# Kernel tuning notes

Measured on AMD Instinct MI355X. Metric: run time of the kernel, lower is better.

Reference implementation:

```python
import jax, jax.numpy as jnp
import numpy as np

N_HEADS = 4
D_K = 64


def setup_inputs() -> dict:
    key = jax.random.key(0)
    k1, k2, k3, k4, k5 = jax.random.split(key, 5)
    C = 256
    return {
        "x": jax.random.normal(k1, (16, C, 32, 32), dtype=jnp.float32),
        "W_qkv": jax.random.normal(k2, (C, N_HEADS * D_K * 3), dtype=jnp.float32) * (C ** -0.5),
        "b_qkv": jax.random.normal(k3, (N_HEADS * D_K * 3,), dtype=jnp.float32) * 0.02,
        "W_out": jax.random.normal(k4, (N_HEADS * D_K, C), dtype=jnp.float32) * ((N_HEADS * D_K) ** -0.5),
        "b_out": jax.random.normal(k5, (C,), dtype=jnp.float32) * 0.02,
    }


def reference(x, W_qkv, b_qkv, W_out, b_out):
    # NOTE: the original forward never applies self.norm and ignores t.
    B, C, H, W = x.shape
    N = H * W
    scale = D_K ** -0.5
    xf = x.reshape(B, C, N).transpose(0, 2, 1)            # [B, N, C]
    qkv = (xf @ W_qkv + b_qkv).reshape(B, N, N_HEADS, 3 * D_K)
    q, k, v = jnp.split(qkv, 3, axis=-1)                  # each [B, N, H, dk]
    attn = jnp.einsum('bihd,bjhd->bijh', q, k) * scale    # [B, N, N, H]
    attn = jax.nn.softmax(attn, axis=2)                   # softmax over keys (j)
    res = jnp.einsum('bijh,bjhd->bihd', attn, v)          # [B, N, H, dk]
    res = res.reshape(B, N, N_HEADS * D_K)
    res = res @ W_out + b_out + xf                        # residual on flattened x
    return res.transpose(0, 2, 1).reshape(B, C, H, W)
```

## Files before the change

### kernel.cpp

```cpp
#include <hip/hip_runtime.h>
#include <math.h>

#define NN 1024

typedef __attribute__((ext_vector_type(8))) __bf16 bf16x8;
typedef __attribute__((ext_vector_type(4))) __bf16 bf16x4;
typedef __attribute__((ext_vector_type(4))) float f32x4;

__device__ __forceinline__ unsigned short f2bf(float f) {
    __bf16 h = (__bf16)f;
    return *(unsigned short*)&h;
}
__device__ __forceinline__ ushort4 pack4(float a, float b, float c, float d) {
    bf16x4 v;
    v[0] = (__bf16)a; v[1] = (__bf16)b; v[2] = (__bf16)c; v[3] = (__bf16)d;
    return *(ushort4*)&v;
}
__device__ __forceinline__ float bf2f(unsigned short u) {
    unsigned v = (unsigned)u << 16;
    return __uint_as_float(v);
}

__device__ __forceinline__ void async_cp16(const unsigned short* g, unsigned short* l) {
    __builtin_amdgcn_global_load_lds(
        (const __attribute__((address_space(1))) unsigned int*)g,
        (__attribute__((address_space(3))) unsigned int*)l,
        16, 0, 0);
}

__global__ __launch_bounds__(256) void prep_transpose(
    const float* __restrict__ x, const float* __restrict__ Wq,
    const float* __restrict__ Wo,
    unsigned short* __restrict__ xb, unsigned short* __restrict__ Wqt,
    unsigned short* __restrict__ Wot)
{
    __shared__ __align__(16) unsigned short T[64 * 72];
    const int bx = blockIdx.x;
    const int rt = blockIdx.y;
    const float* src; unsigned short* dst; int ncol, c0;
    if (bx < 256) {
        int b = bx >> 4; int ct = bx & 15;
        src = x + (size_t)b * 256 * 1024; dst = xb + (size_t)b * 1024 * 256;
        ncol = 1024; c0 = ct * 64;
    } else if (bx < 268) {
        src = Wq; dst = Wqt; ncol = 768; c0 = (bx - 256) * 64;
    } else {
        src = Wo; dst = Wot; ncol = 256; c0 = (bx - 268) * 64;
    }
    const int t = threadIdx.x;
    #pragma unroll
    for (int i = 0; i < 4; ++i) {
        int r  = i * 16 + (t >> 4);
        int c4 = (t & 15) * 4;
        float4 v = *(const float4*)&src[(size_t)(rt * 64 + r) * ncol + c0 + c4];
        *(ushort4*)&T[r * 72 + c4] = pack4(v.x, v.y, v.z, v.w);
    }
    __syncthreads();
    #pragma unroll
    for (int i = 0; i < 2; ++i) {
        int task = t + 256 * i;
        int c = task & 63, rs = task >> 6;
        ushort u8[8];
        #pragma unroll
        for (int k = 0; k < 8; ++k) u8[k] = T[(rs * 8 + k) * 72 + c];
        *(uint4*)&dst[(size_t)(c0 + c) * 256 + rt * 64 + rs * 8] = *(uint4*)u8;
    }
}

__global__ __launch_bounds__(256, 4) void qkv_gemm(
    const unsigned short* __restrict__ xb, const unsigned short* __restrict__ Wqt,
    const float* __restrict__ bias,
    unsigned short* __restrict__ Qb, unsigned short* __restrict__ Kb,
    unsigned short* __restrict__ Vtb)
{
    __shared__ __align__(16) unsigned short As[128 * 40];
    __shared__ __align__(16) unsigned short Bs[128 * 40];
    const int jt = blockIdx.x;
    const int m0 = blockIdx.y * 128;
    const int b  = m0 >> 10;
    const int n0 = m0 & 1023;
    const int t = threadIdx.x;
    const int w = t >> 6, lane = t & 63, quad = lane >> 4, cc = lane & 15;
    const int wm = (w & 1) * 64;
    const int wj = (w >> 1) * 64;

    f32x4 acc[4][4];
    #pragma unroll
    for (int ms = 0; ms < 4; ++ms)
        #pragma unroll
        for (int js = 0; js < 4; ++js) acc[ms][js] = (f32x4)(0.f);

    for (int k0 = 0; k0 < 256; k0 += 32) {
        __syncthreads();
        #pragma unroll
        for (int i = 0; i < 2; ++i) {
            int flat = t + 256 * i;
            int row = flat >> 2, seg = flat & 3;
            *(uint4*)&As[row * 40 + seg * 8] =
                *(const uint4*)&xb[(size_t)(m0 + row) * 256 + k0 + seg * 8];
            *(uint4*)&Bs[row * 40 + seg * 8] =
                *(const uint4*)&Wqt[(size_t)(jt * 128 + row) * 256 + k0 + seg * 8];
        }
        __syncthreads();
        bf16x8 af[4], bfr[4];
        #pragma unroll
        for (int ms = 0; ms < 4; ++ms)
            af[ms] = *(bf16x8*)&As[(wm + ms * 16 + cc) * 40 + quad * 8];
        #pragma unroll
        for (int js = 0; js < 4; ++js)
            bfr[js] = *(bf16x8*)&Bs[(wj + js * 16 + cc) * 40 + quad * 8];
        #pragma unroll
        for (int ms = 0; ms < 4; ++ms)
            #pragma unroll
            for (int js = 0; js < 4; ++js)
                acc[ms][js] = __builtin_amdgcn_mfma_f32_16x16x32_bf16(
                    af[ms], bfr[js], acc[ms][js], 0, 0, 0);
    }

    const int chunk = jt * 2 + (w >> 1);
    const int h = chunk / 3, type = chunk % 3;
    const size_t bh = (size_t)b * 4 + h;
    float bias_r[4];
    #pragma unroll
    for (int js = 0; js < 4; ++js) bias_r[js] = bias[jt * 128 + wj + js * 16 + cc];

    if (type == 2) {
        #pragma unroll
        for (int ms = 0; ms < 4; ++ms)
            #pragma unroll
            for (int js = 0; js < 4; ++js) {
                int dd = js * 16 + cc;
                int n = n0 + wm + ms * 16 + quad * 4;
                *(ushort4*)&Vtb[(bh * 64 + dd) * NN + n] =
                    pack4(acc[ms][js][0] + bias_r[js], acc[ms][js][1] + bias_r[js],
                          acc[ms][js][2] + bias_r[js], acc[ms][js][3] + bias_r[js]);
            }
    } else {
        unsigned short* dst = type ? Kb : Qb;
        const float sc = type ? 1.0f : 0.18033688011112042f;
        #pragma unroll
        for (int ms = 0; ms < 4; ++ms)
            #pragma unroll
            for (int js = 0; js < 4; ++js)
                #pragma unroll
                for (int r = 0; r < 4; ++r) {
                    int n = n0 + wm + ms * 16 + quad * 4 + r;
                    dst[(bh * NN + n) * 64 + js * 16 + cc] =
                        f2bf((acc[ms][js][r] + bias_r[js]) * sc);
                }
    }
}

__global__ __launch_bounds__(256, 4) void flash_attn(
    const unsigned short* __restrict__ Qb, const unsigned short* __restrict__ Kb,
    const unsigned short* __restrict__ Vtb, unsigned short* __restrict__ resb)
{
    __shared__ __align__(16) unsigned short QP[4096];
    __shared__ __align__(16) unsigned short Ks0[4096];
    __shared__ __align__(16) unsigned short Ks1[4096];
    __shared__ __align__(16) unsigned short Vt0[4096];
    __shared__ __align__(16) unsigned short Vt1[4096];

    const int blk = blockIdx.x;
    const int qt = blk & 15;
    const int h  = (blk >> 4) & 3;
    const int b  = blk >> 6;
    const int t  = threadIdx.x;
    const int w  = t >> 6;
    const int lane = t & 63;
    const int quad = lane >> 4;
    const int c    = lane & 15;

    const size_t bh = (size_t)(b * 4 + h);
    const unsigned short* Qg = Qb  + bh * NN * 64;
    const unsigned short* Kg = Kb  + bh * NN * 64;
    const unsigned short* Vg = Vtb + bh * 64 * NN;

    #pragma unroll
    for (int i = 0; i < 2; ++i) {
        int f = i * 256 + t;
        int row = f >> 3;
        int gc  = (f & 7) ^ (row & 7);
        async_cp16(&Qg[(size_t)(qt * 64 + row) * 64 + gc * 8], &QP[f * 8]);
        async_cp16(&Kg[(size_t)row * 64 + gc * 8], &Ks0[f * 8]);
        async_cp16(&Vg[(size_t)row * NN + gc * 8], &Vt0[f * 8]);
    }
    __syncthreads();

    bf16x8 qf[2];
    #pragma unroll
    for (int ks = 0; ks < 2; ++ks) {
        int sc_ = (ks * 4 + quad) ^ (c & 7);
        qf[ks] = *(bf16x8*)&QP[((w * 16 + c) * 8 + sc_) * 8];
    }

    float l_part = 0.f;
    f32x4 O[4];
    #pragma unroll
    for (int dt = 0; dt < 4; ++dt) O[dt] = (f32x4)(0.f);

    auto step = [&](int kt, const unsigned short* curK, const unsigned short* curV,
                    unsigned short* nxtK, unsigned short* nxtV,
                    bool pref, bool bar) {
        if (bar) __syncthreads();
        if (pref) {
            int ktn = kt + 1;
            #pragma unroll
            for (int i = 0; i < 2; ++i) {
                int f = i * 256 + t;
                int row = f >> 3;
                int gc  = (f & 7) ^ (row & 7);
                async_cp16(&Kg[(size_t)(ktn * 64 + row) * 64 + gc * 8], &nxtK[f * 8]);
                async_cp16(&Vg[(size_t)row * NN + ktn * 64 + gc * 8], &nxtV[f * 8]);
            }
        }

        f32x4 S[4];
        #pragma unroll
        for (int jt = 0; jt < 4; ++jt) S[jt] = (f32x4)(0.f);
        #pragma unroll
        for (int ks = 0; ks < 2; ++ks) {
            #pragma unroll
            for (int jt = 0; jt < 4; ++jt) {
                int sc_ = (ks * 4 + quad) ^ (c & 7);
                bf16x8 kf = *(bf16x8*)&curK[((jt * 16 + c) * 8 + sc_) * 8];
                S[jt] = __builtin_amdgcn_mfma_f32_16x16x32_bf16(kf, qf[ks], S[jt], 0, 0, 0);
            }
        }

        float p[4][4], rsj[4];
        #pragma unroll
        for (int jt = 0; jt < 4; ++jt) {
            #pragma unroll
            for (int r = 0; r < 4; ++r)
                p[jt][r] = __builtin_amdgcn_exp2f(S[jt][r]);
            rsj[jt] = (p[jt][0] + p[jt][1]) + (p[jt][2] + p[jt][3]);
        }
        l_part += (rsj[0] + rsj[1]) + (rsj[2] + rsj[3]);

        #pragma unroll
        for (int jt = 0; jt < 4; ++jt) {
            int scw = (jt * 2 + (quad >> 1)) ^ (c & 7);
            *(ushort4*)&QP[(w * 16 + c) * 64 + scw * 8 + (quad & 1) * 4] =
                pack4(p[jt][0], p[jt][1], p[jt][2], p[jt][3]);
        }

        #pragma unroll
        for (int js = 0; js < 2; ++js) {
            int scp = (js * 4 + quad) ^ (c & 7);
            bf16x8 pf = *(bf16x8*)&QP[(w * 16 + c) * 64 + scp * 8];
            #pragma unroll
            for (int dt = 0; dt < 4; ++dt) {
                int sc_ = (js * 4 + quad) ^ (c & 7);
                bf16x8 vf = *(bf16x8*)&curV[((dt * 16 + c) * 8 + sc_) * 8];
                O[dt] = __builtin_amdgcn_mfma_f32_16x16x32_bf16(pf, vf, O[dt], 0, 0, 0);
            }
        }
    };

    step(0, Ks0, Vt0, Ks1, Vt1, true, false);
    for (int kt2 = 0; kt2 < 7; ++kt2) {
        int kt = 2 * kt2 + 1;
        step(kt,     Ks1, Vt1, Ks0, Vt0, true, true);
        step(kt + 1, Ks0, Vt0, Ks1, Vt1, true, true);
    }
    step(15, Ks1, Vt1, Ks0, Vt0, false, true);

    float l_tot = l_part;
    l_tot += __shfl_xor(l_tot, 16);
    l_tot += __shfl_xor(l_tot, 32);

    float linv[4];
    #pragma unroll
    for (int r = 0; r < 4; ++r) linv[r] = 1.f / __shfl(l_tot, quad * 4 + r);
    #pragma unroll
    for (int dt = 0; dt < 4; ++dt)
        #pragma unroll
        for (int r = 0; r < 4; ++r) {
            int row = qt * 64 + w * 16 + quad * 4 + r;
            resb[((size_t)(b * NN + row)) * 256 + h * 64 + dt * 16 + c] =
                f2bf(O[dt][r] * linv[r]);
        }
}

__global__ __launch_bounds__(256, 4) void out_gemm(
    const unsigned short* __restrict__ resb, const unsigned short* __restrict__ Wot,
    const float* __restrict__ bias, const unsigned short* __restrict__ xb,
    float* __restrict__ out)
{
    __shared__ __align__(16) unsigned short As[64 * 40];
    __shared__ __align__(16) unsigned short Bs[64 * 40];
    const int n0 = blockIdx.x * 64;
    const int c0 = blockIdx.y * 64;
    const int b  = blockIdx.z;
    const int t = threadIdx.x;
    const int w = t >> 6, lane = t & 63, quad = lane >> 4, cc = lane & 15;
    const int wm = (w & 1) * 32;
    const int wj = (w >> 1) * 32;

    f32x4 acc[2][2];
    #pragma unroll
    for (int ms = 0; ms < 2; ++ms)
        #pragma unroll
        for (int js = 0; js < 2; ++js) acc[ms][js] = (f32x4)(0.f);

    for (int k0 = 0; k0 < 256; k0 += 32) {
        __syncthreads();
        {
            int r = t >> 2, seg = t & 3;
            *(uint4*)&As[r * 40 + seg * 8] =
                *(const uint4*)&resb[((size_t)b * NN + n0 + r) * 256 + k0 + seg * 8];
            *(uint4*)&Bs[r * 40 + seg * 8] =
                *(const uint4*)&Wot[(size_t)(c0 + r) * 256 + k0 + seg * 8];
        }
        __syncthreads();
        bf16x8 af[2], bfr[2];
        #pragma unroll
        for (int ms = 0; ms < 2; ++ms)
            af[ms] = *(bf16x8*)&As[(wm + ms * 16 + cc) * 40 + quad * 8];
        #pragma unroll
        for (int js = 0; js < 2; ++js)
            bfr[js] = *(bf16x8*)&Bs[(wj + js * 16 + cc) * 40 + quad * 8];
        #pragma unroll
        for (int ms = 0; ms < 2; ++ms)
            #pragma unroll
            for (int js = 0; js < 2; ++js)
                acc[ms][js] = __builtin_amdgcn_mfma_f32_16x16x32_bf16(
                    af[ms], bfr[js], acc[ms][js], 0, 0, 0);
    }

    #pragma unroll
    for (int js = 0; js < 2; ++js) {
        int cI = c0 + wj + js * 16 + cc;
        float bi = bias[cI];
        #pragma unroll
        for (int ms = 0; ms < 2; ++ms) {
            int n = n0 + wm + ms * 16 + quad * 4;
            size_t off = ((size_t)b * 256 + cI) * NN + n;
            float4 o;
            float* op = &o.x;
            #pragma unroll
            for (int r = 0; r < 4; ++r) {
                float xr = bf2f(xb[((size_t)b * NN + n + r) * 256 + cI]);
                op[r] = acc[ms][js][r] + bi + xr;
            }
            *(float4*)&out[off] = o;
        }
    }
}

extern "C" void kernel_launch(void* const* d_in, const int* in_sizes, int n_in,
                              void* d_out, int out_size, void* d_ws, size_t ws_size,
                              hipStream_t stream)
{
    const float* x     = (const float*)d_in[0];
    const float* W_qkv = (const float*)d_in[1];
    const float* b_qkv = (const float*)d_in[2];
    const float* W_out = (const float*)d_in[3];
    const float* b_out = (const float*)d_in[4];
    float* out = (float*)d_out;

    char* wsc = (char*)d_ws;
    unsigned short* xb   = (unsigned short*)(wsc);
    unsigned short* Wqt  = (unsigned short*)(wsc + ((size_t)8 << 20));
    unsigned short* Wot  = (unsigned short*)(wsc + ((size_t)8 << 20) + ((size_t)512 << 10));
    unsigned short* Qb   = (unsigned short*)(wsc + ((size_t)9  << 20));
    unsigned short* Kb   = (unsigned short*)(wsc + ((size_t)17 << 20));
    unsigned short* Vtb  = (unsigned short*)(wsc + ((size_t)25 << 20));
    unsigned short* resb = (unsigned short*)(wsc + ((size_t)33 << 20));

    prep_transpose<<<dim3(272, 4), 256, 0, stream>>>(x, W_qkv, W_out, xb, Wqt, Wot);
    qkv_gemm<<<dim3(6, 128), 256, 0, stream>>>(xb, Wqt, b_qkv, Qb, Kb, Vtb);
    flash_attn<<<dim3(1024), 256, 0, stream>>>(Qb, Kb, Vtb, resb);
    out_gemm<<<dim3(16, 4, 16), 256, 0, stream>>>(resb, Wot, b_out, xb, out);
}
```

Measured before the change: 130.3 us.

## Split flash-attention warps across query and key halves, reducing partial outputs in LDS

Each of the four waves previously owned 16 query rows and covered all 64 keys of a tile. Now the waves form a 2x2 grid: each owns 32 query rows and half of the key tile. Each K fragment feeds two MFMAs and each V fragment feeds two, which halves LDS fragment reads per MFMA. The cost is a final cross-wave reduction of the partial O and row sums through LDS, an extra barrier, and twice the accumulator registers per wave.

```diff
diff --git a/kernel.cpp b/kernel.cpp
--- a/kernel.cpp
+++ b/kernel.cpp
@@ -155,11 +155,12 @@
     const unsigned short* __restrict__ Qb, const unsigned short* __restrict__ Kb,
     const unsigned short* __restrict__ Vtb, unsigned short* __restrict__ resb)
 {
-    __shared__ __align__(16) unsigned short QP[4096];
-    __shared__ __align__(16) unsigned short Ks0[4096];
-    __shared__ __align__(16) unsigned short Ks1[4096];
-    __shared__ __align__(16) unsigned short Vt0[4096];
-    __shared__ __align__(16) unsigned short Vt1[4096];
+    __shared__ __align__(16) unsigned short LDS[5 * 4096];
+    unsigned short* QP  = LDS;
+    unsigned short* Ks0 = LDS + 4096;
+    unsigned short* Ks1 = LDS + 2 * 4096;
+    unsigned short* Vt0 = LDS + 3 * 4096;
+    unsigned short* Vt1 = LDS + 4 * 4096;
 
     const int blk = blockIdx.x;
     const int qt = blk & 15;
@@ -170,6 +171,8 @@
     const int lane = t & 63;
     const int quad = lane >> 4;
     const int c    = lane & 15;
+    const int qh = w & 1;
+    const int jh = w >> 1;
 
     const size_t bh = (size_t)(b * 4 + h);
     const unsigned short* Qg = Qb  + bh * NN * 64;
@@ -187,17 +190,22 @@
     }
     __syncthreads();
 
-    bf16x8 qf[2];
-    #pragma unroll
-    for (int ks = 0; ks < 2; ++ks) {
-        int sc_ = (ks * 4 + quad) ^ (c & 7);
-        qf[ks] = *(bf16x8*)&QP[((w * 16 + c) * 8 + sc_) * 8];
-    }
-
-    float l_part = 0.f;
-    f32x4 O[4];
-    #pragma unroll
-    for (int dt = 0; dt < 4; ++dt) O[dt] = (f32x4)(0.f);
+    bf16x8 qf[2][2];
+    #pragma unroll
+    for (int u = 0; u < 2; ++u)
+        #pragma unroll
+        for (int ks = 0; ks < 2; ++ks) {
+            int sc_ = (ks * 4 + quad) ^ (c & 7);
+            qf[u][ks] = *(bf16x8*)&QP[((qh * 32 + u * 16 + c) * 8 + sc_) * 8];
+        }
+    __syncthreads();
+
+    float l_part[2] = {0.f, 0.f};
+    f32x4 O[2][4];
+    #pragma unroll
+    for (int u = 0; u < 2; ++u)
+        #pragma unroll
+        for (int dt = 0; dt < 4; ++dt) O[u][dt] = (f32x4)(0.f);
 
     auto step = [&](int kt, const unsigned short* curK, const unsigned short* curV,
                     unsigned short* nxtK, unsigned short* nxtV,
@@ -215,46 +223,61 @@
             }
         }
 
-        f32x4 S[4];
-        #pragma unroll
-        for (int jt = 0; jt < 4; ++jt) S[jt] = (f32x4)(0.f);
+        f32x4 S[2][2];
+        #pragma unroll
+        for (int u = 0; u < 2; ++u)
+            #pragma unroll
+            for (int jt = 0; jt < 2; ++jt) S[u][jt] = (f32x4)(0.f);
         #pragma unroll
         for (int ks = 0; ks < 2; ++ks) {
             #pragma unroll
-            for (int jt = 0; jt < 4; ++jt) {
+            for (int jt = 0; jt < 2; ++jt) {
                 int sc_ = (ks * 4 + quad) ^ (c & 7);
-                bf16x8 kf = *(bf16x8*)&curK[((jt * 16 + c) * 8 + sc_) * 8];
-                S[jt] = __builtin_amdgcn_mfma_f32_16x16x32_bf16(kf, qf[ks], S[jt], 0, 0, 0);
-            }
-        }
-
-        float p[4][4], rsj[4];
-        #pragma unroll
-        for (int jt = 0; jt < 4; ++jt) {
-            #pragma unroll
-            for (int r = 0; r < 4; ++r)
-                p[jt][r] = __builtin_amdgcn_exp2f(S[jt][r]);
-            rsj[jt] = (p[jt][0] + p[jt][1]) + (p[jt][2] + p[jt][3]);
-        }
-        l_part += (rsj[0] + rsj[1]) + (rsj[2] + rsj[3]);
-
-        #pragma unroll
-        for (int jt = 0; jt < 4; ++jt) {
-            int scw = (jt * 2 + (quad >> 1)) ^ (c & 7);
-            *(ushort4*)&QP[(w * 16 + c) * 64 + scw * 8 + (quad & 1) * 4] =
-                pack4(p[jt][0], p[jt][1], p[jt][2], p[jt][3]);
-        }
-
-        #pragma unroll
-        for (int js = 0; js < 2; ++js) {
-            int scp = (js * 4 + quad) ^ (c & 7);
-            bf16x8 pf = *(bf16x8*)&QP[(w * 16 + c) * 64 + scp * 8];
-            #pragma unroll
-            for (int dt = 0; dt < 4; ++dt) {
-                int sc_ = (js * 4 + quad) ^ (c & 7);
-                bf16x8 vf = *(bf16x8*)&curV[((dt * 16 + c) * 8 + sc_) * 8];
-                O[dt] = __builtin_amdgcn_mfma_f32_16x16x32_bf16(pf, vf, O[dt], 0, 0, 0);
-            }
+                bf16x8 kf = *(bf16x8*)&curK[((jh * 32 + jt * 16 + c) * 8 + sc_) * 8];
+                #pragma unroll
+                for (int u = 0; u < 2; ++u)
+                    S[u][jt] = __builtin_amdgcn_mfma_f32_16x16x32_bf16(
+                        kf, qf[u][ks], S[u][jt], 0, 0, 0);
+            }
+        }
+
+        float p[2][2][4];
+        #pragma unroll
+        for (int u = 0; u < 2; ++u) {
+            float rsj[2];
+            #pragma unroll
+            for (int jt = 0; jt < 2; ++jt) {
+                #pragma unroll
+                for (int r = 0; r < 4; ++r)
+                    p[u][jt][r] = __builtin_amdgcn_exp2f(S[u][jt][r]);
+                rsj[jt] = (p[u][jt][0] + p[u][jt][1]) + (p[u][jt][2] + p[u][jt][3]);
+            }
+            l_part[u] += rsj[0] + rsj[1];
+        }
+
+        #pragma unroll
+        for (int u = 0; u < 2; ++u)
+            #pragma unroll
+            for (int jt = 0; jt < 2; ++jt) {
+                int chunkj = jh * 4 + jt * 2 + (quad >> 1);
+                *(ushort4*)&QP[(qh * 32 + u * 16 + c) * 64 +
+                               (chunkj ^ (c & 7)) * 8 + (quad & 1) * 4] =
+                    pack4(p[u][jt][0], p[u][jt][1], p[u][jt][2], p[u][jt][3]);
+            }
+
+        bf16x8 pf[2];
+        #pragma unroll
+        for (int u = 0; u < 2; ++u)
+            pf[u] = *(bf16x8*)&QP[(qh * 32 + u * 16 + c) * 64 +
+                                  ((jh * 4 + quad) ^ (c & 7)) * 8];
+        #pragma unroll
+        for (int dt = 0; dt < 4; ++dt) {
+            bf16x8 vf = *(bf16x8*)&curV[((dt * 16 + c) * 8 +
+                                         ((jh * 4 + quad) ^ (c & 7))) * 8];
+            #pragma unroll
+            for (int u = 0; u < 2; ++u)
+                O[u][dt] = __builtin_amdgcn_mfma_f32_16x16x32_bf16(
+                    pf[u], vf, O[u][dt], 0, 0, 0);
         }
     };
 
@@ -266,21 +289,48 @@
     }
     step(15, Ks1, Vt1, Ks0, Vt0, false, true);
 
-    float l_tot = l_part;
-    l_tot += __shfl_xor(l_tot, 16);
-    l_tot += __shfl_xor(l_tot, 32);
-
-    float linv[4];
-    #pragma unroll
-    for (int r = 0; r < 4; ++r) linv[r] = 1.f / __shfl(l_tot, quad * 4 + r);
-    #pragma unroll
-    for (int dt = 0; dt < 4; ++dt)
-        #pragma unroll
-        for (int r = 0; r < 4; ++r) {
-            int row = qt * 64 + w * 16 + quad * 4 + r;
-            resb[((size_t)(b * NN + row)) * 256 + h * 64 + dt * 16 + c] =
-                f2bf(O[dt][r] * linv[r]);
-        }
+    #pragma unroll
+    for (int u = 0; u < 2; ++u) {
+        l_part[u] += __shfl_xor(l_part[u], 16);
+        l_part[u] += __shfl_xor(l_part[u], 32);
+    }
+
+    __syncthreads();
+    float* Oscr = (float*)(LDS + 4096);
+    float* Lbuf = (float*)LDS;
+
+    if (jh == 1) {
+        #pragma unroll
+        for (int u = 0; u < 2; ++u) {
+            #pragma unroll
+            for (int dt = 0; dt < 4; ++dt)
+                #pragma unroll
+                for (int r = 0; r < 4; ++r)
+                    Oscr[(qh * 32 + u * 16 + quad * 4 + r) * 64 + dt * 16 + c] =
+                        O[u][dt][r];
+            Lbuf[64 + qh * 32 + u * 16 + c] = l_part[u];
+        }
+    }
+    __syncthreads();
+    if (jh == 0) {
+        #pragma unroll
+        for (int u = 0; u < 2; ++u) {
+            float l_tot = l_part[u] + Lbuf[64 + qh * 32 + u * 16 + c];
+            float linv[4];
+            #pragma unroll
+            for (int r = 0; r < 4; ++r) linv[r] = 1.f / __shfl(l_tot, quad * 4 + r);
+            #pragma unroll
+            for (int dt = 0; dt < 4; ++dt)
+                #pragma unroll
+                for (int r = 0; r < 4; ++r) {
+                    float o = O[u][dt][r] +
+                        Oscr[(qh * 32 + u * 16 + quad * 4 + r) * 64 + dt * 16 + c];
+                    int row = qt * 64 + qh * 32 + u * 16 + quad * 4 + r;
+                    resb[((size_t)(b * NN + row)) * 256 + h * 64 + dt * 16 + c] =
+                        f2bf(o * linv[r]);
+                }
+        }
+    }
 }
 
 __global__ __launch_bounds__(256, 4) void out_gemm(
```

After: 132.0 us. No clear change (+1.3%).

## Double-buffer QKV and output GEMMs with async LDS loads and swizzled tiles

Applied to the files above, without the earlier changes.

Rewrites the K-loop of both projection GEMMs to load 64-wide K tiles into two LDS buffers with async global-to-LDS copies, so the next tile's load overlaps the current tile's MFMA work. It also replaces the padded LDS layout with an XOR swizzle to avoid bank conflicts. The QKV GEMM's launch bound drops to 2 blocks per CU to make room for the larger shared memory. This adds LDS pressure and lowers occupancy, and only the GEMM stages change while attention likely dominates runtime.

```diff
diff --git a/kernel.cpp b/kernel.cpp
--- a/kernel.cpp
+++ b/kernel.cpp
@@ -67,14 +67,14 @@
     }
 }
 
-__global__ __launch_bounds__(256, 4) void qkv_gemm(
+__global__ __launch_bounds__(256, 2) void qkv_gemm(
     const unsigned short* __restrict__ xb, const unsigned short* __restrict__ Wqt,
     const float* __restrict__ bias,
     unsigned short* __restrict__ Qb, unsigned short* __restrict__ Kb,
     unsigned short* __restrict__ Vtb)
 {
-    __shared__ __align__(16) unsigned short As[128 * 40];
-    __shared__ __align__(16) unsigned short Bs[128 * 40];
+    __shared__ __align__(16) unsigned short As[2][8192];
+    __shared__ __align__(16) unsigned short Bs[2][8192];
     const int jt = blockIdx.x;
     const int m0 = blockIdx.y * 128;
     const int b  = m0 >> 10;
@@ -90,31 +90,48 @@
         #pragma unroll
         for (int js = 0; js < 4; ++js) acc[ms][js] = (f32x4)(0.f);
 
-    for (int k0 = 0; k0 < 256; k0 += 32) {
-        __syncthreads();
-        #pragma unroll
-        for (int i = 0; i < 2; ++i) {
-            int flat = t + 256 * i;
-            int row = flat >> 2, seg = flat & 3;
-            *(uint4*)&As[row * 40 + seg * 8] =
-                *(const uint4*)&xb[(size_t)(m0 + row) * 256 + k0 + seg * 8];
-            *(uint4*)&Bs[row * 40 + seg * 8] =
-                *(const uint4*)&Wqt[(size_t)(jt * 128 + row) * 256 + k0 + seg * 8];
-        }
-        __syncthreads();
-        bf16x8 af[4], bfr[4];
-        #pragma unroll
-        for (int ms = 0; ms < 4; ++ms)
-            af[ms] = *(bf16x8*)&As[(wm + ms * 16 + cc) * 40 + quad * 8];
-        #pragma unroll
-        for (int js = 0; js < 4; ++js)
-            bfr[js] = *(bf16x8*)&Bs[(wj + js * 16 + cc) * 40 + quad * 8];
-        #pragma unroll
-        for (int ms = 0; ms < 4; ++ms)
-            #pragma unroll
-            for (int js = 0; js < 4; ++js)
-                acc[ms][js] = __builtin_amdgcn_mfma_f32_16x16x32_bf16(
-                    af[ms], bfr[js], acc[ms][js], 0, 0, 0);
+    auto stage = [&](int k0, unsigned short* dA, unsigned short* dB) {
+        #pragma unroll
+        for (int i = 0; i < 4; ++i) {
+            int f = i * 256 + t;
+            int row = f >> 3;
+            int gc  = (f & 7) ^ (row & 7);
+            async_cp16(&xb[(size_t)(m0 + row) * 256 + k0 + gc * 8], &dA[f * 8]);
+            async_cp16(&Wqt[(size_t)(jt * 128 + row) * 256 + k0 + gc * 8], &dB[f * 8]);
+        }
+    };
+
+    stage(0, As[0], Bs[0]);
+    __syncthreads();
+
+    #pragma unroll
+    for (int s = 0; s < 4; ++s) {
+        const int cur = s & 1;
+        if (s > 0) __syncthreads();
+        if (s < 3) stage((s + 1) * 64, As[cur ^ 1], Bs[cur ^ 1]);
+
+        #pragma unroll
+        for (int ks = 0; ks < 2; ++ks) {
+            bf16x8 af[4], bfr[4];
+            #pragma unroll
+            for (int ms = 0; ms < 4; ++ms) {
+                int row = wm + ms * 16 + cc;
+                int sc = (ks * 4 + quad) ^ (cc & 7);
+                af[ms] = *(bf16x8*)&As[cur][row * 64 + sc * 8];
+            }
+            #pragma unroll
+            for (int js = 0; js < 4; ++js) {
+                int row = wj + js * 16 + cc;
+                int sc = (ks * 4 + quad) ^ (cc & 7);
+                bfr[js] = *(bf16x8*)&Bs[cur][row * 64 + sc * 8];
+            }
+            #pragma unroll
+            for (int ms = 0; ms < 4; ++ms)
+                #pragma unroll
+                for (int js = 0; js < 4; ++js)
+                    acc[ms][js] = __builtin_amdgcn_mfma_f32_16x16x32_bf16(
+                        af[ms], bfr[js], acc[ms][js], 0, 0, 0);
+        }
     }
 
     const int chunk = jt * 2 + (w >> 1);
@@ -288,8 +305,8 @@
     const float* __restrict__ bias, const unsigned short* __restrict__ xb,
     float* __restrict__ out)
 {
-    __shared__ __align__(16) unsigned short As[64 * 40];
-    __shared__ __align__(16) unsigned short Bs[64 * 40];
+    __shared__ __align__(16) unsigned short As[2][4096];
+    __shared__ __align__(16) unsigned short Bs[2][4096];
     const int n0 = blockIdx.x * 64;
     const int c0 = blockIdx.y * 64;
     const int b  = blockIdx.z;
@@ -304,29 +321,48 @@
         #pragma unroll
         for (int js = 0; js < 2; ++js) acc[ms][js] = (f32x4)(0.f);
 
-    for (int k0 = 0; k0 < 256; k0 += 32) {
-        __syncthreads();
-        {
-            int r = t >> 2, seg = t & 3;
-            *(uint4*)&As[r * 40 + seg * 8] =
-                *(const uint4*)&resb[((size_t)b * NN + n0 + r) * 256 + k0 + seg * 8];
-            *(uint4*)&Bs[r * 40 + seg * 8] =
-                *(const uint4*)&Wot[(size_t)(c0 + r) * 256 + k0 + seg * 8];
-        }
-        __syncthreads();
-        bf16x8 af[2], bfr[2];
-        #pragma unroll
-        for (int ms = 0; ms < 2; ++ms)
-            af[ms] = *(bf16x8*)&As[(wm + ms * 16 + cc) * 40 + quad * 8];
-        #pragma unroll
-        for (int js = 0; js < 2; ++js)
-            bfr[js] = *(bf16x8*)&Bs[(wj + js * 16 + cc) * 40 + quad * 8];
-        #pragma unroll
-        for (int ms = 0; ms < 2; ++ms)
-            #pragma unroll
-            for (int js = 0; js < 2; ++js)
-                acc[ms][js] = __builtin_amdgcn_mfma_f32_16x16x32_bf16(
-                    af[ms], bfr[js], acc[ms][js], 0, 0, 0);
+    auto stage = [&](int k0, unsigned short* dA, unsigned short* dB) {
+        #pragma unroll
+        for (int i = 0; i < 2; ++i) {
+            int f = i * 256 + t;
+            int row = f >> 3;
+            int gc  = (f & 7) ^ (row & 7);
+            async_cp16(&resb[((size_t)b * NN + n0 + row) * 256 + k0 + gc * 8], &dA[f * 8]);
+            async_cp16(&Wot[(size_t)(c0 + row) * 256 + k0 + gc * 8], &dB[f * 8]);
+        }
+    };
+
+    stage(0, As[0], Bs[0]);
+    __syncthreads();
+
+    #pragma unroll
+    for (int s = 0; s < 4; ++s) {
+        const int cur = s & 1;
+        if (s > 0) __syncthreads();
+        if (s < 3) stage((s + 1) * 64, As[cur ^ 1], Bs[cur ^ 1]);
+
+        #pragma unroll
+        for (int ks = 0; ks < 2; ++ks) {
+            bf16x8 af[2], bfr[2];
+            #pragma unroll
+            for (int ms = 0; ms < 2; ++ms) {
+                int row = wm + ms * 16 + cc;
+                int sc = (ks * 4 + quad) ^ (cc & 7);
+                af[ms] = *(bf16x8*)&As[cur][row * 64 + sc * 8];
+            }
+            #pragma unroll
+            for (int js = 0; js < 2; ++js) {
+                int row = wj + js * 16 + cc;
+                int sc = (ks * 4 + quad) ^ (cc & 7);
+                bfr[js] = *(bf16x8*)&Bs[cur][row * 64 + sc * 8];
+            }
+            #pragma unroll
+            for (int ms = 0; ms < 2; ++ms)
+                #pragma unroll
+                for (int js = 0; js < 2; ++js)
+                    acc[ms][js] = __builtin_amdgcn_mfma_f32_16x16x32_bf16(
+                        af[ms], bfr[js], acc[ms][js], 0, 0, 0);
+        }
     }
 
     #pragma unroll
```

Result: no change. 131.3 us (+0.8%).
